# Kernel tuning notes

Hardware: AMD Instinct MI355X
Metric: run time of the kernel (lower is better)

Reference implementation:

```python
import jax, jax.numpy as jnp
import numpy as np

DIM = 1024
NUM_HEADS = 16
HEAD_DIM = DIM // NUM_HEADS


def setup_inputs() -> dict:
    key = jax.random.key(0)
    ks = jax.random.split(key, 16)
    B, Sx, Sy = 4, 1024, 1024
    s = 1.0 / np.sqrt(DIM)
    inp = {
        'x': jax.random.normal(ks[0], (B, Sx, DIM), dtype=jnp.float32),
        'y': jax.random.normal(ks[1], (B, Sy, DIM), dtype=jnp.float32),
    }
    names = ['Kx', 'Qx', 'Vx', 'Ky', 'Vy', 'out']
    for i, n in enumerate(names):
        inp[f'W_{n}'] = jax.random.uniform(ks[2 + 2 * i], (DIM, DIM), dtype=jnp.float32, minval=-s, maxval=s)
        inp[f'b_{n}'] = jax.random.uniform(ks[3 + 2 * i], (DIM,), dtype=jnp.float32, minval=-s, maxval=s)
    return inp


def _heads(t, B, S):
    # [B, S, DIM] -> [B, H, S, Dh]
    return t.reshape(B, S, NUM_HEADS, HEAD_DIM).transpose(0, 2, 1, 3)


def _attn(x, y, W_Kx, b_Kx, W_Qx, b_Qx, W_Vx, b_Vx, W_Ky, b_Ky, W_Vy, b_Vy, W_out, b_out):
    B, Sx, _ = x.shape
    Sy = y.shape[1]
    lin = lambda t, W, b: t @ W.T + b
    Q = _heads(lin(x, W_Qx, b_Qx), B, Sx)
    Kc = jnp.concatenate([_heads(lin(x, W_Kx, b_Kx), B, Sx), _heads(lin(y, W_Ky, b_Ky), B, Sy)], axis=2)
    Vc = jnp.concatenate([_heads(lin(x, W_Vx, b_Vx), B, Sx), _heads(lin(y, W_Vy, b_Vy), B, Sy)], axis=2)
    scores = jnp.einsum('bhqd,bhkd->bhqk', Q, Kc) / np.sqrt(HEAD_DIM).astype(np.float32)
    w = jax.nn.softmax(scores, axis=-1)
    o = jnp.einsum('bhqk,bhkd->bhqd', w, Vc)  # [B, H, Sx, Dh]
    o = o.transpose(0, 2, 1, 3).reshape(B, Sx, DIM)
    return lin(o, W_out, b_out)


def reference(x, y, W_Kx, b_Kx, W_Qx, b_Qx, W_Vx, b_Vx, W_Ky, b_Ky, W_Vy, b_Vy, W_out, b_out):
    return _attn(x, y, W_Kx, b_Kx, W_Qx, b_Qx, W_Vx, b_Vx, W_Ky, b_Ky, W_Vy, b_Vy, W_out, b_out)
```

## Files before the change

kernel.cpp:

```cpp
#include <hip/hip_runtime.h>

#define DIMN 1024
#define NH 16
#define DH 64
#define SXX 1024
#define SKV 2048

typedef __bf16 bf16x8 __attribute__((ext_vector_type(8)));
typedef float f32x4 __attribute__((ext_vector_type(4)));
typedef unsigned short us8 __attribute__((ext_vector_type(8)));

__device__ __forceinline__ unsigned short f2bs(float f) {
    return (unsigned short)((__builtin_bit_cast(unsigned int, f) + 0x8000u) >> 16);
}
__device__ __forceinline__ void gl_lds16(const void* g, void* l) {
    __builtin_amdgcn_global_load_lds(
        (const __attribute__((address_space(1))) unsigned int*)g,
        (__attribute__((address_space(3))) unsigned int*)l, 16, 0, 0);
}

struct CvtArgs {
    const float* src[8];
    unsigned short* dst[8];
    int start[8];
};
__global__ __launch_bounds__(256) void cvt_all(CvtArgs a) {
    int b = blockIdx.x;
    int r = 0;
#pragma unroll
    for (int i = 1; i < 8; i++) r += (b >= a.start[i]);
    int off = ((b - a.start[r]) * 256 + (int)threadIdx.x) * 8;
    const float* s = a.src[r] + off;
    float4 f0 = *(const float4*)(s);
    float4 f1 = *(const float4*)(s + 4);
    us8 o;
    o[0] = f2bs(f0.x); o[1] = f2bs(f0.y); o[2] = f2bs(f0.z); o[3] = f2bs(f0.w);
    o[4] = f2bs(f1.x); o[5] = f2bs(f1.y); o[6] = f2bs(f1.z); o[7] = f2bs(f1.w);
    *(us8*)(a.dst[r] + off) = o;
}

__device__ __forceinline__ void gemm_core(const unsigned short* __restrict__ A,
                                          const unsigned short* __restrict__ W,
                                          unsigned short* As, unsigned short* Bs,
                                          int m0, int n0, f32x4 (&acc)[4][4]) {
    const int K = DIMN;
    int tid = threadIdx.x, wave = tid >> 6, lane = tid & 63;
    int l15 = lane & 15, quad = lane >> 4;
    int wm = wave >> 1, wn = wave & 1;
    int srow = wave * 8 + (lane >> 3);
    int gcol = ((lane & 7) ^ (lane >> 3)) * 8;
    const unsigned short* gA = A + (size_t)(m0 + srow) * K + gcol;
    const unsigned short* gW = W + (size_t)(n0 + srow) * K + gcol;
    unsigned short* lA = As + wave * 512;
    unsigned short* lB = Bs + wave * 512;
    int slot0 = (quad ^ (l15 & 7)) * 8;

    for (int k0 = 0; k0 < K; k0 += 64) {
        if (k0) __syncthreads();
#pragma unroll
        for (int j = 0; j < 4; j++) {
            gl_lds16(gA + k0 + (size_t)j * 32 * K, lA + j * 2048);
            gl_lds16(gW + k0 + (size_t)j * 32 * K, lB + j * 2048);
        }
        __syncthreads();
#pragma unroll
        for (int kk = 0; kk < 2; kk++) {
            int sl = slot0 ^ (kk * 32);
            bf16x8 af[4], bf[4];
#pragma unroll
            for (int mi = 0; mi < 4; mi++)
                af[mi] = __builtin_bit_cast(bf16x8, *(const us8*)(&As[(wm * 64 + mi * 16 + l15) * 64 + sl]));
#pragma unroll
            for (int ni = 0; ni < 4; ni++)
                bf[ni] = __builtin_bit_cast(bf16x8, *(const us8*)(&Bs[(wn * 64 + ni * 16 + l15) * 64 + sl]));
#pragma unroll
            for (int mi = 0; mi < 4; mi++)
#pragma unroll
                for (int ni = 0; ni < 4; ni++)
                    acc[mi][ni] = __builtin_amdgcn_mfma_f32_16x16x32_bf16(af[mi], bf[ni], acc[mi][ni], 0, 0, 0);
        }
    }
}

__global__ __launch_bounds__(256, 2) void gemm_kq(
        const unsigned short* __restrict__ xb, const unsigned short* __restrict__ yb,
        const unsigned short* __restrict__ Wb,
        const float* __restrict__ b_Kx, const float* __restrict__ b_Qx, const float* __restrict__ b_Ky,
        unsigned short* __restrict__ Qd, unsigned short* __restrict__ Kd, float qscale) {
    __shared__ __align__(16) unsigned short As[128 * 64];
    __shared__ __align__(16) unsigned short Bs[128 * 64];
    int which = blockIdx.x >> 3;
    int n0 = (blockIdx.x & 7) * 128, m0 = blockIdx.y * 128;
    const unsigned short* A = (which == 2) ? yb : xb;
    const unsigned short* W = Wb + (size_t)((which == 0) ? 0 : (which == 1) ? 1 : 3) * 1048576;
    const float* bp = (which == 0) ? b_Kx : (which == 1) ? b_Qx : b_Ky;
    int roff = (which == 2) ? 1024 : 0;
    float sc = (which == 1) ? qscale : 1.0f;

    f32x4 acc[4][4] = {};
    gemm_core(A, W, As, Bs, m0, n0, acc);

    int tid = threadIdx.x, wave = tid >> 6, lane = tid & 63;
    int l15 = lane & 15, quad = lane >> 4;
    int wm = wave >> 1, wn = wave & 1;
#pragma unroll
    for (int mi = 0; mi < 4; mi++) {
        int mbase = m0 + wm * 64 + mi * 16 + quad * 4;
#pragma unroll
        for (int ni = 0; ni < 4; ni++) {
            int n = n0 + wn * 64 + ni * 16 + l15;
            float bv = bp[n];
            int h = n >> 6, d = n & 63;
#pragma unroll
            for (int r = 0; r < 4; r++) {
                float v = (acc[mi][ni][r] + bv) * sc;
                int mm = mbase + r;
                int bidx = mm >> 10, s = mm & 1023;
                if (which == 1)
                    Qd[((size_t)(bidx * NH + h) * SXX + s) * DH + d] = f2bs(v);
                else
                    Kd[((size_t)(bidx * NH + h) * SKV + s + roff) * DH + d] = f2bs(v);
            }
        }
    }
}

__global__ __launch_bounds__(256, 2) void gemm_v(
        const unsigned short* __restrict__ xb, const unsigned short* __restrict__ yb,
        const unsigned short* __restrict__ Wb,
        const float* __restrict__ b_Vx, const float* __restrict__ b_Vy,
        unsigned short* __restrict__ Vd) {
    __shared__ __align__(16) unsigned short As[128 * 64];
    __shared__ __align__(16) unsigned short Bs[128 * 64];
    int side = blockIdx.y >> 3;
    int m0 = (blockIdx.y & 7) * 128, n0 = blockIdx.x * 128;
    const unsigned short* Wv = Wb + (size_t)(side ? 4 : 2) * 1048576;
    const unsigned short* act = side ? yb : xb;
    const float* bp = side ? b_Vy : b_Vx;
    int roff = side ? 1024 : 0;

    f32x4 acc[4][4] = {};
    gemm_core(Wv, act, As, Bs, m0, n0, acc);

    int tid = threadIdx.x, wave = tid >> 6, lane = tid & 63;
    int l15 = lane & 15, quad = lane >> 4;
    int wm = wave >> 1, wn = wave & 1;
#pragma unroll
    for (int mi = 0; mi < 4; mi++) {
        int mbase = m0 + wm * 64 + mi * 16 + quad * 4;
#pragma unroll
        for (int ni = 0; ni < 4; ni++) {
            int n = n0 + wn * 64 + ni * 16 + l15;
            int bidx = n >> 10, s = n & 1023;
#pragma unroll
            for (int r = 0; r < 4; r++) {
                int m = mbase + r;
                int h = m >> 6, d = m & 63;
                float v = acc[mi][ni][r] + bp[m];
                Vd[((size_t)(bidx * NH + h) * DH + d) * SKV + s + roff] = f2bs(v);
            }
        }
    }
}

__global__ __launch_bounds__(256, 2) void gemm_out(
        const unsigned short* __restrict__ Ob, const unsigned short* __restrict__ Wo,
        const float* __restrict__ bo, float* __restrict__ outp) {
    __shared__ __align__(16) unsigned short As[128 * 64];
    __shared__ __align__(16) unsigned short Bs[128 * 64];
    int n0 = blockIdx.x * 128, m0 = blockIdx.y * 128;
    f32x4 acc[4][4] = {};
    gemm_core(Ob, Wo, As, Bs, m0, n0, acc);

    int tid = threadIdx.x, wave = tid >> 6, lane = tid & 63;
    int l15 = lane & 15, quad = lane >> 4;
    int wm = wave >> 1, wn = wave & 1;
#pragma unroll
    for (int mi = 0; mi < 4; mi++) {
        int mbase = m0 + wm * 64 + mi * 16 + quad * 4;
#pragma unroll
        for (int ni = 0; ni < 4; ni++) {
            int n = n0 + wn * 64 + ni * 16 + l15;
            float bv = bo[n];
#pragma unroll
            for (int r = 0; r < 4; r++)
                outp[(size_t)(mbase + r) * DIMN + n] = acc[mi][ni][r] + bv;
        }
    }
}

__global__ __launch_bounds__(256, 2) void flash_attn(
        const unsigned short* __restrict__ Qb,
        const unsigned short* __restrict__ Kc,
        const unsigned short* __restrict__ Vt,
        unsigned short* __restrict__ Ob) {
    __shared__ __align__(16) unsigned short Ks[2][64 * 64];
    __shared__ __align__(16) unsigned short Vs[2][64 * 64];
    __shared__ __align__(16) unsigned short Ps[4][32 * 64];
    int tid = threadIdx.x, wave = tid >> 6, lane = tid & 63;
    int l15 = lane & 15, quad = lane >> 4;
    int bh = blockIdx.x;
    int qbase = blockIdx.y * 128 + wave * 32;

    const unsigned short* Qp = Qb + ((size_t)bh * SXX + qbase) * DH;
    bf16x8 bq[2][2];
#pragma unroll
    for (int qt = 0; qt < 2; qt++) {
        bq[qt][0] = __builtin_bit_cast(bf16x8, *(const us8*)(&Qp[(qt * 16 + l15) * DH + quad * 8]));
        bq[qt][1] = __builtin_bit_cast(bf16x8, *(const us8*)(&Qp[(qt * 16 + l15) * DH + 32 + quad * 8]));
    }

    const unsigned short* Kg = Kc + (size_t)bh * SKV * DH;
    const unsigned short* Vg = Vt + (size_t)bh * DH * SKV;

    int srow_lo = 8 * wave + (lane >> 3);
    int srow_hi = srow_lo + 32;
    int swz = ((lane & 7) ^ (lane >> 3)) * 8;
    int sl = (lane & 7) * 8;

    us8 pk0, pk1, pv0, pv1;
    auto gload = [&](int c) {
        pk0 = *(const us8*)(Kg + (size_t)(c + srow_lo) * DH + swz);
        pk1 = *(const us8*)(Kg + (size_t)(c + srow_hi) * DH + swz);
        pv0 = *(const us8*)(Vg + (size_t)srow_lo * SKV + c + swz);
        pv1 = *(const us8*)(Vg + (size_t)srow_hi * SKV + c + swz);
    };
    auto lstore = [&](int buf) {
        *(us8*)(&Ks[buf][srow_lo * 64 + sl]) = pk0;
        *(us8*)(&Ks[buf][srow_hi * 64 + sl]) = pk1;
        *(us8*)(&Vs[buf][srow_lo * 64 + sl]) = pv0;
        *(us8*)(&Vs[buf][srow_hi * 64 + sl]) = pv1;
    };

    f32x4 o[2][4] = {};
    float lsum[2] = {0.f, 0.f};
    int cA = (quad ^ (l15 & 7)) * 8;

    gload(0);
    lstore(0);
    __syncthreads();

    for (int c = 0; c < SKV; c += 64) {
        int cur = (c >> 6) & 1;
        bool more = (c + 64) < SKV;
        if (more) gload(c + 64);

        const unsigned short* ks = &Ks[cur][0];
        bf16x8 ak0[4], ak1[4];
#pragma unroll
        for (int ni = 0; ni < 4; ni++) {
            int row = (ni * 16 + l15) * 64;
            ak0[ni] = __builtin_bit_cast(bf16x8, *(const us8*)(ks + row + cA));
            ak1[ni] = __builtin_bit_cast(bf16x8, *(const us8*)(ks + row + (cA ^ 32)));
        }

        unsigned short* pw = &Ps[wave][0];
#pragma unroll
        for (int qt = 0; qt < 2; qt++) {
#pragma unroll
            for (int ni = 0; ni < 4; ni++) {
                f32x4 z = {};
                z = __builtin_amdgcn_mfma_f32_16x16x32_bf16(ak0[ni], bq[qt][0], z, 0, 0, 0);
                z = __builtin_amdgcn_mfma_f32_16x16x32_bf16(ak1[ni], bq[qt][1], z, 0, 0, 0);
                float p0 = __builtin_amdgcn_exp2f(z[0]);
                float p1 = __builtin_amdgcn_exp2f(z[1]);
                float p2 = __builtin_amdgcn_exp2f(z[2]);
                float p3 = __builtin_amdgcn_exp2f(z[3]);
                lsum[qt] += (p0 + p1) + (p2 + p3);
                unsigned int lo = ((__builtin_bit_cast(unsigned int, p0) + 0x8000u) >> 16)
                                | ((__builtin_bit_cast(unsigned int, p1) + 0x8000u) & 0xffff0000u);
                unsigned int hi = ((__builtin_bit_cast(unsigned int, p2) + 0x8000u) >> 16)
                                | ((__builtin_bit_cast(unsigned int, p3) + 0x8000u) & 0xffff0000u);
                int c8p = (2 * ni + (quad >> 1)) ^ (l15 & 7);
                *(uint2*)(pw + (qt * 16 + l15) * 64 + c8p * 8 + (quad & 1) * 4) = make_uint2(lo, hi);
            }
        }

        const unsigned short* vs = &Vs[cur][0];
        bf16x8 av0[4], av1[4];
#pragma unroll
        for (int ni = 0; ni < 4; ni++) {
            int row = (ni * 16 + l15) * 64;
            av0[ni] = __builtin_bit_cast(bf16x8, *(const us8*)(vs + row + cA));
            av1[ni] = __builtin_bit_cast(bf16x8, *(const us8*)(vs + row + (cA ^ 32)));
        }
#pragma unroll
        for (int qt = 0; qt < 2; qt++) {
            bf16x8 ap0 = __builtin_bit_cast(bf16x8, *(const us8*)(pw + (qt * 16 + l15) * 64 + cA));
            bf16x8 ap1 = __builtin_bit_cast(bf16x8, *(const us8*)(pw + (qt * 16 + l15) * 64 + (cA ^ 32)));
#pragma unroll
            for (int ni = 0; ni < 4; ni++) {
                o[qt][ni] = __builtin_amdgcn_mfma_f32_16x16x32_bf16(ap0, av0[ni], o[qt][ni], 0, 0, 0);
                o[qt][ni] = __builtin_amdgcn_mfma_f32_16x16x32_bf16(ap1, av1[ni], o[qt][ni], 0, 0, 0);
            }
        }

        if (more) lstore(1 - cur);
        __syncthreads();
    }

    int b = bh >> 4, h = bh & 15;
#pragma unroll
    for (int qt = 0; qt < 2; qt++) {
        float ls = lsum[qt];
        ls += __shfl_xor(ls, 16);
        ls += __shfl_xor(ls, 32);
#pragma unroll
        for (int r = 0; r < 4; r++) {
            float lt = __shfl(ls, quad * 4 + r);
            float inv = __builtin_amdgcn_rcpf(lt);
            int q = qbase + qt * 16 + quad * 4 + r;
#pragma unroll
            for (int ni = 0; ni < 4; ni++)
                Ob[((size_t)b * SXX + q) * DIMN + h * DH + ni * 16 + l15] = f2bs(o[qt][ni][r] * inv);
        }
    }
}

extern "C" void kernel_launch(void* const* d_in, const int* in_sizes, int n_in,
                              void* d_out, int out_size, void* d_ws, size_t ws_size,
                              hipStream_t stream) {
    (void)in_sizes; (void)n_in; (void)out_size; (void)ws_size;
    const float* x     = (const float*)d_in[0];
    const float* y     = (const float*)d_in[1];
    const float* W_Kx  = (const float*)d_in[2];
    const float* b_Kx  = (const float*)d_in[3];
    const float* W_Qx  = (const float*)d_in[4];
    const float* b_Qx  = (const float*)d_in[5];
    const float* W_Vx  = (const float*)d_in[6];
    const float* b_Vx  = (const float*)d_in[7];
    const float* W_Ky  = (const float*)d_in[8];
    const float* b_Ky  = (const float*)d_in[9];
    const float* W_Vy  = (const float*)d_in[10];
    const float* b_Vy  = (const float*)d_in[11];
    const float* W_out = (const float*)d_in[12];
    const float* b_out = (const float*)d_in[13];
    float* out = (float*)d_out;

    char* ws = (char*)d_ws;
    unsigned short* xb  = (unsigned short*)(ws);
    unsigned short* yb  = (unsigned short*)(ws + (size_t)( 8 << 20));
    unsigned short* Qb  = (unsigned short*)(ws + (size_t)(16 << 20));
    unsigned short* Kcw = (unsigned short*)(ws + (size_t)(24 << 20));
    unsigned short* Vtw = (unsigned short*)(ws + (size_t)(40 << 20));
    unsigned short* Obw = (unsigned short*)(ws + (size_t)(56 << 20));
    unsigned short* Wb  = (unsigned short*)(ws + (size_t)(64 << 20));

    CvtArgs ca;
    ca.src[0] = x;     ca.dst[0] = xb;                 ca.start[0] = 0;
    ca.src[1] = y;     ca.dst[1] = yb;                 ca.start[1] = 2048;
    ca.src[2] = W_Kx;  ca.dst[2] = Wb + 0u * 1048576;  ca.start[2] = 4096;
    ca.src[3] = W_Qx;  ca.dst[3] = Wb + 1u * 1048576;  ca.start[3] = 4608;
    ca.src[4] = W_Vx;  ca.dst[4] = Wb + 2u * 1048576;  ca.start[4] = 5120;
    ca.src[5] = W_Ky;  ca.dst[5] = Wb + 3u * 1048576;  ca.start[5] = 5632;
    ca.src[6] = W_Vy;  ca.dst[6] = Wb + 4u * 1048576;  ca.start[6] = 6144;
    ca.src[7] = W_out; ca.dst[7] = Wb + 5u * 1048576;  ca.start[7] = 6656;
    cvt_all<<<7168, 256, 0, stream>>>(ca);

    const float qscale = 0.125f * 1.44269504088896340736f;
    gemm_kq<<<dim3(24, 32), 256, 0, stream>>>(xb, yb, Wb, b_Kx, b_Qx, b_Ky, Qb, Kcw, qscale);
    gemm_v<<<dim3(32, 16), 256, 0, stream>>>(xb, yb, Wb, b_Vx, b_Vy, Vtw);
    flash_attn<<<dim3(64, 8), 256, 0, stream>>>(Qb, Kcw, Vtw, Obw);
    gemm_out<<<dim3(8, 32), 256, 0, stream>>>(Obw, Wb + 5u * 1048576, b_out, out);
}
```

Baseline: 256.4 us.

## Double-buffer GEMM LDS loads, merge K/Q/V projections, shrink out-proj tiles

The GEMM core now double-buffers its LDS tiles, issuing global-to-LDS loads for the next K-slice while MFMAs run on the current one, with one barrier per iteration instead of two. The K/Q and V projection kernels are merged into a single 1280-block launch, which removes a launch boundary and the tail between them. The output projection switches to 64x128 tiles (512 blocks) so more CUs are occupied. Doubling LDS to 64KB per block may lower occupancy.

```diff
diff --git a/kernel.cpp b/kernel.cpp
--- a/kernel.cpp
+++ b/kernel.cpp
@@ -12,6 +12,10 @@
 
 __device__ __forceinline__ unsigned short f2bs(float f) {
     return (unsigned short)((__builtin_bit_cast(unsigned int, f) + 0x8000u) >> 16);
+}
+__device__ __forceinline__ unsigned int pk2(float a, float b) {
+    return ((__builtin_bit_cast(unsigned int, a) + 0x8000u) >> 16)
+         | ((__builtin_bit_cast(unsigned int, b) + 0x8000u) & 0xffff0000u);
 }
 __device__ __forceinline__ void gl_lds16(const void* g, void* l) {
     __builtin_amdgcn_global_load_lds(
@@ -51,28 +55,36 @@
     int gcol = ((lane & 7) ^ (lane >> 3)) * 8;
     const unsigned short* gA = A + (size_t)(m0 + srow) * K + gcol;
     const unsigned short* gW = W + (size_t)(n0 + srow) * K + gcol;
-    unsigned short* lA = As + wave * 512;
-    unsigned short* lB = Bs + wave * 512;
+    int ldsoff = wave * 512;
     int slot0 = (quad ^ (l15 & 7)) * 8;
 
-    for (int k0 = 0; k0 < K; k0 += 64) {
-        if (k0) __syncthreads();
+    auto stage = [&](int buf, int k0) {
+        unsigned short* lA = As + buf * 8192 + ldsoff;
+        unsigned short* lB = Bs + buf * 8192 + ldsoff;
 #pragma unroll
         for (int j = 0; j < 4; j++) {
             gl_lds16(gA + k0 + (size_t)j * 32 * K, lA + j * 2048);
             gl_lds16(gW + k0 + (size_t)j * 32 * K, lB + j * 2048);
         }
+    };
+
+    stage(0, 0);
+    for (int k0 = 0; k0 < K; k0 += 64) {
+        int buf = (k0 >> 6) & 1;
         __syncthreads();
+        if (k0 + 64 < K) stage(buf ^ 1, k0 + 64);
+        const unsigned short* as = As + buf * 8192;
+        const unsigned short* bs = Bs + buf * 8192;
 #pragma unroll
         for (int kk = 0; kk < 2; kk++) {
             int sl = slot0 ^ (kk * 32);
             bf16x8 af[4], bf[4];
 #pragma unroll
             for (int mi = 0; mi < 4; mi++)
-                af[mi] = __builtin_bit_cast(bf16x8, *(const us8*)(&As[(wm * 64 + mi * 16 + l15) * 64 + sl]));
+                af[mi] = __builtin_bit_cast(bf16x8, *(const us8*)(&as[(wm * 64 + mi * 16 + l15) * 64 + sl]));
 #pragma unroll
             for (int ni = 0; ni < 4; ni++)
-                bf[ni] = __builtin_bit_cast(bf16x8, *(const us8*)(&Bs[(wn * 64 + ni * 16 + l15) * 64 + sl]));
+                bf[ni] = __builtin_bit_cast(bf16x8, *(const us8*)(&bs[(wn * 64 + ni * 16 + l15) * 64 + sl]));
 #pragma unroll
             for (int mi = 0; mi < 4; mi++)
 #pragma unroll
@@ -82,102 +94,141 @@
     }
 }
 
-__global__ __launch_bounds__(256, 2) void gemm_kq(
+__global__ __launch_bounds__(256, 2) void gemm_proj(
         const unsigned short* __restrict__ xb, const unsigned short* __restrict__ yb,
         const unsigned short* __restrict__ Wb,
         const float* __restrict__ b_Kx, const float* __restrict__ b_Qx, const float* __restrict__ b_Ky,
-        unsigned short* __restrict__ Qd, unsigned short* __restrict__ Kd, float qscale) {
-    __shared__ __align__(16) unsigned short As[128 * 64];
-    __shared__ __align__(16) unsigned short Bs[128 * 64];
-    int which = blockIdx.x >> 3;
-    int n0 = (blockIdx.x & 7) * 128, m0 = blockIdx.y * 128;
-    const unsigned short* A = (which == 2) ? yb : xb;
-    const unsigned short* W = Wb + (size_t)((which == 0) ? 0 : (which == 1) ? 1 : 3) * 1048576;
-    const float* bp = (which == 0) ? b_Kx : (which == 1) ? b_Qx : b_Ky;
-    int roff = (which == 2) ? 1024 : 0;
-    float sc = (which == 1) ? qscale : 1.0f;
-
-    f32x4 acc[4][4] = {};
-    gemm_core(A, W, As, Bs, m0, n0, acc);
-
+        const float* __restrict__ b_Vx, const float* __restrict__ b_Vy,
+        unsigned short* __restrict__ Qd, unsigned short* __restrict__ Kd,
+        unsigned short* __restrict__ Vd, float qscale) {
+    __shared__ __align__(16) unsigned short As[2 * 128 * 64];
+    __shared__ __align__(16) unsigned short Bs[2 * 128 * 64];
+    int bx = blockIdx.x;
     int tid = threadIdx.x, wave = tid >> 6, lane = tid & 63;
     int l15 = lane & 15, quad = lane >> 4;
     int wm = wave >> 1, wn = wave & 1;
-#pragma unroll
-    for (int mi = 0; mi < 4; mi++) {
-        int mbase = m0 + wm * 64 + mi * 16 + quad * 4;
-#pragma unroll
-        for (int ni = 0; ni < 4; ni++) {
-            int n = n0 + wn * 64 + ni * 16 + l15;
-            float bv = bp[n];
-            int h = n >> 6, d = n & 63;
-#pragma unroll
-            for (int r = 0; r < 4; r++) {
-                float v = (acc[mi][ni][r] + bv) * sc;
-                int mm = mbase + r;
-                int bidx = mm >> 10, s = mm & 1023;
-                if (which == 1)
-                    Qd[((size_t)(bidx * NH + h) * SXX + s) * DH + d] = f2bs(v);
-                else
-                    Kd[((size_t)(bidx * NH + h) * SKV + s + roff) * DH + d] = f2bs(v);
+
+    f32x4 acc[4][4] = {};
+
+    if (bx < 768) {
+        int sub = bx >> 8, t = bx & 255;
+        int n0 = (t & 7) * 128, m0 = (t >> 3) * 128;
+        const unsigned short* A = (sub == 2) ? yb : xb;
+        const unsigned short* W = Wb + (size_t)((sub == 0) ? 0 : (sub == 1) ? 1 : 3) * 1048576;
+        const float* bp = (sub == 0) ? b_Kx : (sub == 1) ? b_Qx : b_Ky;
+        int roff = (sub == 2) ? 1024 : 0;
+        float sc = (sub == 1) ? qscale : 1.0f;
+
+        gemm_core(A, W, As, Bs, m0, n0, acc);
+
+#pragma unroll
+        for (int mi = 0; mi < 4; mi++) {
+            int mbase = m0 + wm * 64 + mi * 16 + quad * 4;
+#pragma unroll
+            for (int ni = 0; ni < 4; ni++) {
+                int n = n0 + wn * 64 + ni * 16 + l15;
+                float bv = bp[n];
+                int h = n >> 6, d = n & 63;
+#pragma unroll
+                for (int r = 0; r < 4; r++) {
+                    float v = (acc[mi][ni][r] + bv) * sc;
+                    int mm = mbase + r;
+                    int bidx = mm >> 10, s = mm & 1023;
+                    if (sub == 1)
+                        Qd[((size_t)(bidx * NH + h) * SXX + s) * DH + d] = f2bs(v);
+                    else
+                        Kd[((size_t)(bidx * NH + h) * SKV + s + roff) * DH + d] = f2bs(v);
+                }
             }
         }
-    }
-}
-
-__global__ __launch_bounds__(256, 2) void gemm_v(
-        const unsigned short* __restrict__ xb, const unsigned short* __restrict__ yb,
-        const unsigned short* __restrict__ Wb,
-        const float* __restrict__ b_Vx, const float* __restrict__ b_Vy,
-        unsigned short* __restrict__ Vd) {
-    __shared__ __align__(16) unsigned short As[128 * 64];
-    __shared__ __align__(16) unsigned short Bs[128 * 64];
-    int side = blockIdx.y >> 3;
-    int m0 = (blockIdx.y & 7) * 128, n0 = blockIdx.x * 128;
-    const unsigned short* Wv = Wb + (size_t)(side ? 4 : 2) * 1048576;
-    const unsigned short* act = side ? yb : xb;
-    const float* bp = side ? b_Vy : b_Vx;
-    int roff = side ? 1024 : 0;
-
-    f32x4 acc[4][4] = {};
-    gemm_core(Wv, act, As, Bs, m0, n0, acc);
-
+    } else {
+        int u = bx - 768;
+        int side = u >> 8, t = u & 255;
+        int m0 = (t & 7) * 128, n0 = (t >> 3) * 128;
+        const unsigned short* Wv = Wb + (size_t)(side ? 4 : 2) * 1048576;
+        const unsigned short* act = side ? yb : xb;
+        const float* bp = side ? b_Vy : b_Vx;
+        int roff = side ? 1024 : 0;
+
+        gemm_core(Wv, act, As, Bs, m0, n0, acc);
+
+#pragma unroll
+        for (int mi = 0; mi < 4; mi++) {
+            int mbase = m0 + wm * 64 + mi * 16 + quad * 4;
+#pragma unroll
+            for (int ni = 0; ni < 4; ni++) {
+                int n = n0 + wn * 64 + ni * 16 + l15;
+                int bidx = n >> 10, s = n & 1023;
+#pragma unroll
+                for (int r = 0; r < 4; r++) {
+                    int m = mbase + r;
+                    int h = m >> 6, d = m & 63;
+                    float v = acc[mi][ni][r] + bp[m];
+                    Vd[((size_t)(bidx * NH + h) * DH + d) * SKV + s + roff] = f2bs(v);
+                }
+            }
+        }
+    }
+}
+
+__global__ __launch_bounds__(256, 2) void gemm_out(
+        const unsigned short* __restrict__ Ob, const unsigned short* __restrict__ Wo,
+        const float* __restrict__ bo, float* __restrict__ outp) {
+    __shared__ __align__(16) unsigned short As[2 * 64 * 64];
+    __shared__ __align__(16) unsigned short Bs[2 * 128 * 64];
+    const int K = DIMN;
     int tid = threadIdx.x, wave = tid >> 6, lane = tid & 63;
     int l15 = lane & 15, quad = lane >> 4;
     int wm = wave >> 1, wn = wave & 1;
-#pragma unroll
-    for (int mi = 0; mi < 4; mi++) {
-        int mbase = m0 + wm * 64 + mi * 16 + quad * 4;
-#pragma unroll
-        for (int ni = 0; ni < 4; ni++) {
-            int n = n0 + wn * 64 + ni * 16 + l15;
-            int bidx = n >> 10, s = n & 1023;
-#pragma unroll
-            for (int r = 0; r < 4; r++) {
-                int m = mbase + r;
-                int h = m >> 6, d = m & 63;
-                float v = acc[mi][ni][r] + bp[m];
-                Vd[((size_t)(bidx * NH + h) * DH + d) * SKV + s + roff] = f2bs(v);
-            }
-        }
-    }
-}
-
-__global__ __launch_bounds__(256, 2) void gemm_out(
-        const unsigned short* __restrict__ Ob, const unsigned short* __restrict__ Wo,
-        const float* __restrict__ bo, float* __restrict__ outp) {
-    __shared__ __align__(16) unsigned short As[128 * 64];
-    __shared__ __align__(16) unsigned short Bs[128 * 64];
-    int n0 = blockIdx.x * 128, m0 = blockIdx.y * 128;
-    f32x4 acc[4][4] = {};
-    gemm_core(Ob, Wo, As, Bs, m0, n0, acc);
-
-    int tid = threadIdx.x, wave = tid >> 6, lane = tid & 63;
-    int l15 = lane & 15, quad = lane >> 4;
-    int wm = wave >> 1, wn = wave & 1;
-#pragma unroll
-    for (int mi = 0; mi < 4; mi++) {
-        int mbase = m0 + wm * 64 + mi * 16 + quad * 4;
+    int n0 = blockIdx.x * 128, m0 = blockIdx.y * 64;
+
+    int srow = wave * 8 + (lane >> 3);
+    int gcol = ((lane & 7) ^ (lane >> 3)) * 8;
+    const unsigned short* gA = Ob + (size_t)(m0 + srow) * K + gcol;
+    const unsigned short* gW = Wo + (size_t)(n0 + srow) * K + gcol;
+    int ldsoff = wave * 512;
+    int slot0 = (quad ^ (l15 & 7)) * 8;
+
+    auto stage = [&](int buf, int k0) {
+        unsigned short* lA = As + buf * 4096 + ldsoff;
+        unsigned short* lB = Bs + buf * 8192 + ldsoff;
+#pragma unroll
+        for (int j = 0; j < 2; j++)
+            gl_lds16(gA + k0 + (size_t)j * 32 * K, lA + j * 2048);
+#pragma unroll
+        for (int j = 0; j < 4; j++)
+            gl_lds16(gW + k0 + (size_t)j * 32 * K, lB + j * 2048);
+    };
+
+    f32x4 acc[2][4] = {};
+    stage(0, 0);
+    for (int k0 = 0; k0 < K; k0 += 64) {
+        int buf = (k0 >> 6) & 1;
+        __syncthreads();
+        if (k0 + 64 < K) stage(buf ^ 1, k0 + 64);
+        const unsigned short* as = As + buf * 4096;
+        const unsigned short* bs = Bs + buf * 8192;
+#pragma unroll
+        for (int kk = 0; kk < 2; kk++) {
+            int sl = slot0 ^ (kk * 32);
+            bf16x8 af[2], bf[4];
+#pragma unroll
+            for (int mi = 0; mi < 2; mi++)
+                af[mi] = __builtin_bit_cast(bf16x8, *(const us8*)(&as[(wm * 32 + mi * 16 + l15) * 64 + sl]));
+#pragma unroll
+            for (int ni = 0; ni < 4; ni++)
+                bf[ni] = __builtin_bit_cast(bf16x8, *(const us8*)(&bs[(wn * 64 + ni * 16 + l15) * 64 + sl]));
+#pragma unroll
+            for (int mi = 0; mi < 2; mi++)
+#pragma unroll
+                for (int ni = 0; ni < 4; ni++)
+                    acc[mi][ni] = __builtin_amdgcn_mfma_f32_16x16x32_bf16(af[mi], bf[ni], acc[mi][ni], 0, 0, 0);
+        }
+    }
+
+#pragma unroll
+    for (int mi = 0; mi < 2; mi++) {
+        int mbase = m0 + wm * 32 + mi * 16 + quad * 4;
 #pragma unroll
         for (int ni = 0; ni < 4; ni++) {
             int n = n0 + wn * 64 + ni * 16 + l15;
@@ -267,10 +318,8 @@
                 float p2 = __builtin_amdgcn_exp2f(z[2]);
                 float p3 = __builtin_amdgcn_exp2f(z[3]);
                 lsum[qt] += (p0 + p1) + (p2 + p3);
-                unsigned int lo = ((__builtin_bit_cast(unsigned int, p0) + 0x8000u) >> 16)
-                                | ((__builtin_bit_cast(unsigned int, p1) + 0x8000u) & 0xffff0000u);
-                unsigned int hi = ((__builtin_bit_cast(unsigned int, p2) + 0x8000u) >> 16)
-                                | ((__builtin_bit_cast(unsigned int, p3) + 0x8000u) & 0xffff0000u);
+                unsigned int lo = pk2(p0, p1);
+                unsigned int hi = pk2(p2, p3);
                 int c8p = (2 * ni + (quad >> 1)) ^ (l15 & 7);
                 *(uint2*)(pw + (qt * 16 + l15) * 64 + c8p * 8 + (quad & 1) * 4) = make_uint2(lo, hi);
             }
@@ -358,8 +407,8 @@
     cvt_all<<<7168, 256, 0, stream>>>(ca);
 
     const float qscale = 0.125f * 1.44269504088896340736f;
-    gemm_kq<<<dim3(24, 32), 256, 0, stream>>>(xb, yb, Wb, b_Kx, b_Qx, b_Ky, Qb, Kcw, qscale);
-    gemm_v<<<dim3(32, 16), 256, 0, stream>>>(xb, yb, Wb, b_Vx, b_Vy, Vtw);
+    gemm_proj<<<1280, 256, 0, stream>>>(xb, yb, Wb, b_Kx, b_Qx, b_Ky, b_Vx, b_Vy,
+                                        Qb, Kcw, Vtw, qscale);
     flash_attn<<<dim3(64, 8), 256, 0, stream>>>(Qb, Kcw, Vtw, Obw);
-    gemm_out<<<dim3(8, 32), 256, 0, stream>>>(Obw, Wb + 5u * 1048576, b_out, out);
-}
+    gemm_out<<<dim3(8, 64), 256, 0, stream>>>(Obw, Wb + 5u * 1048576, b_out, out);
+}
```

Result: faster. 246.2 us (-4.0%).
